# Kernel tuning notes

Hardware: AMD Instinct MI355X
Metric: run time of the kernel (lower is better)

## Reference

```python
import jax, jax.numpy as jnp
import numpy as np

RANK = 16
ALPHA = 32.0
LORA_SCALE = ALPHA / RANK  # 2.0


def setup_inputs() -> dict:
    key = jax.random.key(0)
    ks = jax.random.split(key, 7)
    B_, S, D_IN, D_OUT = 4, 2048, 4096, 4096
    x = jax.random.normal(ks[0], (B_, S, D_IN), dtype=jnp.float32)
    qweight = jax.random.randint(ks[1], (D_OUT, D_IN), 0, 16, dtype=jnp.int32)
    w_min = jax.random.normal(ks[2], (D_OUT, 1), dtype=jnp.float32) * 0.1
    # row scale ~ (max-min)/15 of typical weights; keep positive
    w_scale = jax.random.uniform(ks[3], (D_OUT, 1), dtype=jnp.float32, minval=1e-3, maxval=0.02)
    bias = jax.random.normal(ks[4], (D_OUT,), dtype=jnp.float32) * 0.02
    A = jax.random.normal(ks[5], (RANK, D_IN), dtype=jnp.float32) * 0.02
    # module inits B to zeros; use small randn so the LoRA branch is exercised
    Bm = jax.random.normal(ks[6], (D_OUT, RANK), dtype=jnp.float32) * 0.02
    return {"x": x, "qweight": qweight, "w_min": w_min, "w_scale": w_scale,
            "bias": bias, "A": A, "B": Bm}


def reference(x, qweight, w_min, w_scale, bias, A, B):
    # Row-wise 4-bit dequant: W[o,i] = q[o,i]*scale[o] + min[o]
    base_weight = qweight.astype(jnp.float32) * w_scale + w_min  # [O, I]
    base_out = jnp.einsum('bsi,oi->bso', x, base_weight) + bias   # [B, S, O]
    # LoRA: (x @ A^T) @ B^T * (alpha/rank); dropout p=0 is identity
    lora_out = jnp.einsum('bsr,or->bso', jnp.einsum('bsi,ri->bsr', x, A), B) * LORA_SCALE
    return base_out + lora_out
```

## Files before the change

kernel.cpp:

```cpp
#include <hip/hip_runtime.h>
#include <hip/hip_bf16.h>

typedef unsigned short u16;
typedef unsigned int u32;
typedef __bf16 bf16x8 __attribute__((ext_vector_type(8)));
typedef float f32x4 __attribute__((ext_vector_type(4)));
typedef u16 u16x4 __attribute__((ext_vector_type(4)));
typedef u16 u16x8 __attribute__((ext_vector_type(8)));

#define D_IN 4096
#define D_OUT 4096
#define M_TOT 8192
#define RANK_ 16

#define BM 256
#define BN 256
#define BK 64
#define NT (D_IN / BK)
#define OPB 2

__device__ __forceinline__ u16 f2bf(float f) {
    union { float f; u32 u; } v; v.f = f;
    u32 u = v.u;
    u32 r = (u + 0x7FFFu + ((u >> 16) & 1u)) >> 16;
    return (u16)r;
}

__global__ __launch_bounds__(256) void dequant_fold_kernel(
        const int* __restrict__ q, const float* __restrict__ wmin,
        const float* __restrict__ wscale, const float* __restrict__ A,
        const float* __restrict__ Bm, u16* __restrict__ Wb) {
    const int K = D_IN;
    int o0 = blockIdx.x * OPB;
    float s0 = wscale[o0], s1 = wscale[o0 + 1];
    float m0 = wmin[o0],   m1 = wmin[o0 + 1];
    float Br0[RANK_], Br1[RANK_];
    #pragma unroll
    for (int r = 0; r < RANK_; ++r) {
        Br0[r] = 2.0f * Bm[(size_t)o0 * RANK_ + r];
        Br1[r] = 2.0f * Bm[(size_t)(o0 + 1) * RANK_ + r];
    }
    for (int i4 = threadIdx.x; i4 < K / 4; i4 += 256) {
        int i = i4 * 4;
        int4 q0 = *(const int4*)(q + (size_t)o0 * K + i);
        int4 q1 = *(const int4*)(q + (size_t)(o0 + 1) * K + i);
        float v00 = (float)q0.x * s0 + m0, v01 = (float)q0.y * s0 + m0;
        float v02 = (float)q0.z * s0 + m0, v03 = (float)q0.w * s0 + m0;
        float v10 = (float)q1.x * s1 + m1, v11 = (float)q1.y * s1 + m1;
        float v12 = (float)q1.z * s1 + m1, v13 = (float)q1.w * s1 + m1;
        #pragma unroll
        for (int r = 0; r < RANK_; ++r) {
            float4 av = *(const float4*)(A + (size_t)r * K + i);
            v00 += Br0[r] * av.x; v01 += Br0[r] * av.y;
            v02 += Br0[r] * av.z; v03 += Br0[r] * av.w;
            v10 += Br1[r] * av.x; v11 += Br1[r] * av.y;
            v12 += Br1[r] * av.z; v13 += Br1[r] * av.w;
        }
        u16x4 o0v, o1v;
        o0v.x = f2bf(v00); o0v.y = f2bf(v01); o0v.z = f2bf(v02); o0v.w = f2bf(v03);
        o1v.x = f2bf(v10); o1v.y = f2bf(v11); o1v.z = f2bf(v12); o1v.w = f2bf(v13);
        *(u16x4*)(Wb + (size_t)o0 * K + i) = o0v;
        *(u16x4*)(Wb + (size_t)(o0 + 1) * K + i) = o1v;
    }
}

__global__ void xcast_kernel(const float* __restrict__ x, u16* __restrict__ xb) {
    size_t i = (size_t)blockIdx.x * blockDim.x + threadIdx.x;
    const float4* p = (const float4*)x + i * 2;
    float4 a = p[0];
    float4 b = p[1];
    u16x8 o;
    o[0] = f2bf(a.x); o[1] = f2bf(a.y); o[2] = f2bf(a.z); o[3] = f2bf(a.w);
    o[4] = f2bf(b.x); o[5] = f2bf(b.y); o[6] = f2bf(b.z); o[7] = f2bf(b.w);
    *(u16x8*)(xb + i * 8) = o;
}


#define STAGE2(srcarr, ldsarr, base, j0, kt) do { _Pragma("unroll") \
    for (int j_ = (j0); j_ < (j0) + 2; ++j_) \
        __builtin_amdgcn_global_load_lds( \
            (__attribute__((address_space(1))) u32*)(srcarr[j_] + (kt) * 64), \
            (__attribute__((address_space(3))) u32*)(smem + (base) + ldsarr[j_]), \
            16, 0, 0); } while (0)

#define MFMA(d, va, vb) d = __builtin_amdgcn_mfma_f32_16x16x32_bf16(va, vb, d, 0, 0, 0)

__global__ __launch_bounds__(512, 2) void gemm_bt_kernel(const u16* __restrict__ Xb,
                                                         const u16* __restrict__ Wb,
                                                         const float* __restrict__ bias,
                                                         float* __restrict__ out) {
    extern __shared__ __align__(16) char smem[];
    const int K = D_IN, N = D_OUT;

    int bid = blockIdx.x;
    int swz = (bid & 7) * 64 + (bid >> 3);
    int tM = swz >> 4;
    int tN = swz & 15;

    int t = threadIdx.x;
    int lane = t & 63;
    int wave = t >> 6;
    int wm = wave >> 2;
    int wn = wave & 3;
    int lr = lane & 15;
    int hi = lane >> 4;
    int l7 = lane & 7;

    int xs0 = ((0 * 4 + hi) ^ l7) << 4;
    int xs1 = ((1 * 4 + hi) ^ l7) << 4;
    int aRow = (wm * 128 + lr) * 128;
    int bRow = (wn * 64 + lr) * 128;

    const u16* srcA[4]; const u16* srcB[4]; int ldsA[4]; int ldsB[4];
    {
        int cA[4] = { t, 1024 + t, 512 + t, 1536 + t };
        int b0 = (t & 255) + ((t >> 8) << 9);
        int cB[4] = { b0, b0 + 1024, b0 + 256, b0 + 1280 };
        #pragma unroll
        for (int j = 0; j < 4; ++j) {
            int ca = cA[j], cb = cB[j];
            int rowa = ca >> 3, rowb = cb >> 3;
            int sa = (ca & 7) ^ (rowa & 7);
            int sb = (cb & 7) ^ (rowb & 7);
            srcA[j] = Xb + (size_t)(tM * 256 + rowa) * K + (sa << 3);
            srcB[j] = Wb + (size_t)(tN * 256 + rowb) * K + (sb << 3);
            ldsA[j] = ca * 16;
            ldsB[j] = cb * 16;
        }
    }

    f32x4 acc[8][4];
    #pragma unroll
    for (int i = 0; i < 8; ++i)
        #pragma unroll
        for (int j = 0; j < 4; ++j)
            acc[i][j] = (f32x4){0.f, 0.f, 0.f, 0.f};

    STAGE2(srcA, ldsA, 0,     0, 0); STAGE2(srcA, ldsA, 0,     2, 0);
    STAGE2(srcB, ldsB, 65536, 0, 0); STAGE2(srcB, ldsB, 65536, 2, 0);
    STAGE2(srcA, ldsA, 32768, 0, 1); STAGE2(srcA, ldsA, 32768, 2, 1);
    STAGE2(srcB, ldsB, 98304, 0, 1); STAGE2(srcB, ldsB, 98304, 2, 1);
    asm volatile("s_waitcnt vmcnt(8)" ::: "memory");
    __builtin_amdgcn_s_barrier();

    bf16x8 a[4][2], b[4][2];

    for (int tt = 0; tt < NT; ++tt) {
        int pA = (tt & 1) * 32768;
        int pB = 65536 + (tt & 1) * 32768;
        bool pre = (tt + 2 < NT);

        #pragma unroll
        for (int mf = 0; mf < 4; ++mf) {
            a[mf][0] = *(const bf16x8*)(smem + pA + aRow + mf * 2048 + xs0);
            a[mf][1] = *(const bf16x8*)(smem + pA + aRow + mf * 2048 + xs1);
        }
        #pragma unroll
        for (int nf = 0; nf < 2; ++nf) {
            b[nf][0] = *(const bf16x8*)(smem + pB + bRow + nf * 2048 + xs0);
            b[nf][1] = *(const bf16x8*)(smem + pB + bRow + nf * 2048 + xs1);
        }
        asm volatile("s_waitcnt lgkmcnt(8)" ::: "memory");
        __builtin_amdgcn_s_barrier();
        asm volatile("s_waitcnt lgkmcnt(0)");
        __builtin_amdgcn_s_setprio(1);
        #pragma unroll
        for (int mf = 0; mf < 4; ++mf)
            #pragma unroll
            for (int nf = 0; nf < 2; ++nf) {
                MFMA(acc[mf][nf], a[mf][0], b[nf][0]);
                MFMA(acc[mf][nf], a[mf][1], b[nf][1]);
            }
        __builtin_amdgcn_s_setprio(0);
        __builtin_amdgcn_s_barrier();

        #pragma unroll
        for (int nf = 2; nf < 4; ++nf) {
            b[nf][0] = *(const bf16x8*)(smem + pB + bRow + nf * 2048 + xs0);
            b[nf][1] = *(const bf16x8*)(smem + pB + bRow + nf * 2048 + xs1);
        }
        if (pre) {
            STAGE2(srcA, ldsA, pA, 0, tt + 2);
            STAGE2(srcB, ldsB, pB, 0, tt + 2);
        }
        __builtin_amdgcn_s_barrier();
        asm volatile("s_waitcnt lgkmcnt(0)");
        __builtin_amdgcn_s_setprio(1);
        #pragma unroll
        for (int mf = 0; mf < 4; ++mf)
            #pragma unroll
            for (int nf = 2; nf < 4; ++nf) {
                MFMA(acc[mf][nf], a[mf][0], b[nf][0]);
                MFMA(acc[mf][nf], a[mf][1], b[nf][1]);
            }
        __builtin_amdgcn_s_setprio(0);
        __builtin_amdgcn_s_barrier();

        #pragma unroll
        for (int mf = 0; mf < 4; ++mf) {
            a[mf][0] = *(const bf16x8*)(smem + pA + aRow + (mf + 4) * 2048 + xs0);
            a[mf][1] = *(const bf16x8*)(smem + pA + aRow + (mf + 4) * 2048 + xs1);
        }
        if (pre) { STAGE2(srcB, ldsB, pB, 2, tt + 2); }
        __builtin_amdgcn_s_barrier();
        asm volatile("s_waitcnt lgkmcnt(0)");
        __builtin_amdgcn_s_setprio(1);
        #pragma unroll
        for (int mf = 0; mf < 4; ++mf)
            #pragma unroll
            for (int nf = 2; nf < 4; ++nf) {
                MFMA(acc[mf + 4][nf], a[mf][0], b[nf][0]);
                MFMA(acc[mf + 4][nf], a[mf][1], b[nf][1]);
            }
        __builtin_amdgcn_s_setprio(0);
        __builtin_amdgcn_s_barrier();

        if (pre) { STAGE2(srcA, ldsA, pA, 2, tt + 2); }
        if (tt < NT - 2) { asm volatile("s_waitcnt vmcnt(8)" ::: "memory"); }
        else             { asm volatile("s_waitcnt vmcnt(0)" ::: "memory"); }
        __builtin_amdgcn_s_barrier();
        __builtin_amdgcn_s_setprio(1);
        #pragma unroll
        for (int mf = 0; mf < 4; ++mf)
            #pragma unroll
            for (int nf = 0; nf < 2; ++nf) {
                MFMA(acc[mf + 4][nf], a[mf][0], b[nf][0]);
                MFMA(acc[mf + 4][nf], a[mf][1], b[nf][1]);
            }
        __builtin_amdgcn_s_setprio(0);
        __builtin_amdgcn_s_barrier();
    }

    #pragma unroll
    for (int nf = 0; nf < 4; ++nf) {
        int gn = tN * 256 + wn * 64 + nf * 16 + lr;
        float bs = bias[gn];
        #pragma unroll
        for (int mf = 0; mf < 8; ++mf) {
            #pragma unroll
            for (int r = 0; r < 4; ++r) {
                int gm = tM * 256 + wm * 128 + mf * 16 + hi * 4 + r;
                out[(size_t)gm * N + gn] = acc[mf][nf][r] + bs;
            }
        }
    }
}

extern "C" void kernel_launch(void* const* d_in, const int* in_sizes, int n_in,
                              void* d_out, int out_size, void* d_ws, size_t ws_size,
                              hipStream_t stream) {
    (void)in_sizes; (void)n_in; (void)out_size; (void)ws_size;
    const float* x      = (const float*)d_in[0];
    const int*   qw     = (const int*)d_in[1];
    const float* wmin   = (const float*)d_in[2];
    const float* wscale = (const float*)d_in[3];
    const float* bias   = (const float*)d_in[4];
    const float* A      = (const float*)d_in[5];
    const float* Bm     = (const float*)d_in[6];
    float* out = (float*)d_out;

    u16* Wb = (u16*)d_ws;
    u16* Xb = Wb + (size_t)D_OUT * D_IN;

    dequant_fold_kernel<<<D_OUT / OPB, 256, 0, stream>>>(qw, wmin, wscale, A, Bm, Wb);
    xcast_kernel<<<(M_TOT * D_IN) / (256 * 8), 256, 0, stream>>>(x, Xb);
    gemm_bt_kernel<<<(M_TOT / BM) * (D_OUT / BN), 512, 131072, stream>>>(Xb, Wb, bias, out);
}
```

Measured before the change: 311.8 us.

## Prefetch next tile's B fragments and regroup staging loads by consumer phase

Reorganizes the main GEMM loop so the B columns 0-1 fragments for the next K-tile are read from LDS during the last MFMA phase of the current tile, with ping-pong register sets and the loop unrolled by two. Global-to-LDS staging is regrouped into row ranges (A rows 0-63/64-127 per wave half, B quarter rows) that match the order in which each phase consumes them, so each refill can be issued as soon as its region is free. The aim is to remove the LDS read latency at the start of each tile and tighten the overlap of async copies with MFMA work, at the cost of more live registers and more complex waitcnt reasoning.

```diff
diff --git a/kernel.cpp b/kernel.cpp
--- a/kernel.cpp
+++ b/kernel.cpp
@@ -76,14 +76,104 @@
 }
 
 
-#define STAGE2(srcarr, ldsarr, base, j0, kt) do { _Pragma("unroll") \
-    for (int j_ = (j0); j_ < (j0) + 2; ++j_) \
+#define STAGE_R(sarr, larr, base, kt) do { _Pragma("unroll") \
+    for (int j_ = 0; j_ < 2; ++j_) \
         __builtin_amdgcn_global_load_lds( \
-            (__attribute__((address_space(1))) u32*)(srcarr[j_] + (kt) * 64), \
-            (__attribute__((address_space(3))) u32*)(smem + (base) + ldsarr[j_]), \
+            (__attribute__((address_space(1))) u32*)(sarr[j_] + (kt) * 64), \
+            (__attribute__((address_space(3))) u32*)(smem + (base) + larr[j_]), \
             16, 0, 0); } while (0)
 
 #define MFMA(d, va, vb) d = __builtin_amdgcn_mfma_f32_16x16x32_bf16(va, vb, d, 0, 0, 0)
+
+#define TILE_BODY(tt, BC, BN_) do { \
+    int pA = ((tt) & 1) * 32768; \
+    int pB = 65536 + ((tt) & 1) * 32768; \
+    int pBn = 65536 + ((~(tt)) & 1) * 32768; \
+    bool pre = ((tt) + 2 < NT); \
+     \
+    _Pragma("unroll") \
+    for (int mf = 0; mf < 4; ++mf) { \
+        a[mf][0] = *(const bf16x8*)(smem + pA + aRow + mf * 2048 + xs0); \
+        a[mf][1] = *(const bf16x8*)(smem + pA + aRow + mf * 2048 + xs1); \
+    } \
+    if (pre && (tt) > 0) { STAGE_R(srcB01, ldsB01, pB, (tt) + 2); } \
+    __builtin_amdgcn_s_barrier(); \
+    asm volatile("s_waitcnt lgkmcnt(0)"); \
+    __builtin_amdgcn_s_setprio(1); \
+    _Pragma("unroll") \
+    for (int mf = 0; mf < 4; ++mf) \
+        _Pragma("unroll") \
+        for (int nf = 0; nf < 2; ++nf) { \
+            MFMA(acc[mf][nf], a[mf][0], BC[nf][0]); \
+            MFMA(acc[mf][nf], a[mf][1], BC[nf][1]); \
+        } \
+    __builtin_amdgcn_s_setprio(0); \
+    __builtin_amdgcn_s_barrier(); \
+     \
+    _Pragma("unroll") \
+    for (int nf = 0; nf < 2; ++nf) { \
+        b23[nf][0] = *(const bf16x8*)(smem + pB + bRow + (nf + 2) * 2048 + xs0); \
+        b23[nf][1] = *(const bf16x8*)(smem + pB + bRow + (nf + 2) * 2048 + xs1); \
+    } \
+    if (pre) { \
+        STAGE_R(srcA03, ldsA03, pA, (tt) + 2); \
+        if ((tt) == 0) { STAGE_R(srcB01, ldsB01, pB, (tt) + 2); } \
+    } \
+    __builtin_amdgcn_s_barrier(); \
+    asm volatile("s_waitcnt lgkmcnt(0)"); \
+    __builtin_amdgcn_s_setprio(1); \
+    _Pragma("unroll") \
+    for (int mf = 0; mf < 4; ++mf) \
+        _Pragma("unroll") \
+        for (int nf = 0; nf < 2; ++nf) { \
+            MFMA(acc[mf][nf + 2], a[mf][0], b23[nf][0]); \
+            MFMA(acc[mf][nf + 2], a[mf][1], b23[nf][1]); \
+        } \
+    __builtin_amdgcn_s_setprio(0); \
+    __builtin_amdgcn_s_barrier(); \
+     \
+    _Pragma("unroll") \
+    for (int mf = 0; mf < 4; ++mf) { \
+        a[mf][0] = *(const bf16x8*)(smem + pA + aRow + (mf + 4) * 2048 + xs0); \
+        a[mf][1] = *(const bf16x8*)(smem + pA + aRow + (mf + 4) * 2048 + xs1); \
+    } \
+    if (pre) { STAGE_R(srcB23, ldsB23, pB, (tt) + 2); } \
+    __builtin_amdgcn_s_barrier(); \
+    asm volatile("s_waitcnt lgkmcnt(0)"); \
+    __builtin_amdgcn_s_setprio(1); \
+    _Pragma("unroll") \
+    for (int mf = 0; mf < 4; ++mf) \
+        _Pragma("unroll") \
+        for (int nf = 0; nf < 2; ++nf) { \
+            MFMA(acc[mf + 4][nf + 2], a[mf][0], b23[nf][0]); \
+            MFMA(acc[mf + 4][nf + 2], a[mf][1], b23[nf][1]); \
+        } \
+    __builtin_amdgcn_s_setprio(0); \
+    __builtin_amdgcn_s_barrier(); \
+     \
+     \
+    if (pre) { STAGE_R(srcA47, ldsA47, pA, (tt) + 2); } \
+    if ((tt) < NT - 2) { asm volatile("s_waitcnt vmcnt(8)" ::: "memory"); } \
+    else               { asm volatile("s_waitcnt vmcnt(0)" ::: "memory"); } \
+    __builtin_amdgcn_s_barrier(); \
+    if ((tt) + 1 < NT) { \
+        _Pragma("unroll") \
+        for (int nf = 0; nf < 2; ++nf) { \
+            BN_[nf][0] = *(const bf16x8*)(smem + pBn + bRow + nf * 2048 + xs0); \
+            BN_[nf][1] = *(const bf16x8*)(smem + pBn + bRow + nf * 2048 + xs1); \
+        } \
+    } \
+    __builtin_amdgcn_s_setprio(1); \
+    _Pragma("unroll") \
+    for (int mf = 0; mf < 4; ++mf) \
+        _Pragma("unroll") \
+        for (int nf = 0; nf < 2; ++nf) { \
+            MFMA(acc[mf + 4][nf], a[mf][0], BC[nf][0]); \
+            MFMA(acc[mf + 4][nf], a[mf][1], BC[nf][1]); \
+        } \
+    __builtin_amdgcn_s_setprio(0); \
+    __builtin_amdgcn_s_barrier(); \
+} while (0)
 
 __global__ __launch_bounds__(512, 2) void gemm_bt_kernel(const u16* __restrict__ Xb,
                                                          const u16* __restrict__ Wb,
@@ -111,22 +201,26 @@
     int aRow = (wm * 128 + lr) * 128;
     int bRow = (wn * 64 + lr) * 128;
 
-    const u16* srcA[4]; const u16* srcB[4]; int ldsA[4]; int ldsB[4];
-    {
-        int cA[4] = { t, 1024 + t, 512 + t, 1536 + t };
-        int b0 = (t & 255) + ((t >> 8) << 9);
-        int cB[4] = { b0, b0 + 1024, b0 + 256, b0 + 1280 };
-        #pragma unroll
-        for (int j = 0; j < 4; ++j) {
-            int ca = cA[j], cb = cB[j];
-            int rowa = ca >> 3, rowb = cb >> 3;
-            int sa = (ca & 7) ^ (rowa & 7);
-            int sb = (cb & 7) ^ (rowb & 7);
-            srcA[j] = Xb + (size_t)(tM * 256 + rowa) * K + (sa << 3);
-            srcB[j] = Wb + (size_t)(tN * 256 + rowb) * K + (sb << 3);
-            ldsA[j] = ca * 16;
-            ldsB[j] = cb * 16;
-        }
+    const u16 *srcA03[2], *srcA47[2], *srcB01[2], *srcB23[2];
+    int ldsA03[2], ldsA47[2], ldsB01[2], ldsB23[2];
+    #pragma unroll
+    for (int j = 0; j < 2; ++j) {
+        int idx = j * 512 + t;
+        int rl = idx >> 3, slot = idx & 7;
+        int rA = (rl & 63) + ((rl >> 6) << 7);
+        int rB = (rl & 31) + ((rl >> 5) << 6);
+        int r = rA;
+        ldsA03[j] = r * 128 + slot * 16;
+        srcA03[j] = Xb + (size_t)(tM * 256 + r) * K + ((slot ^ (r & 7)) << 3);
+        r = rA + 64;
+        ldsA47[j] = r * 128 + slot * 16;
+        srcA47[j] = Xb + (size_t)(tM * 256 + r) * K + ((slot ^ (r & 7)) << 3);
+        r = rB;
+        ldsB01[j] = r * 128 + slot * 16;
+        srcB01[j] = Wb + (size_t)(tN * 256 + r) * K + ((slot ^ (r & 7)) << 3);
+        r = rB + 32;
+        ldsB23[j] = r * 128 + slot * 16;
+        srcB23[j] = Wb + (size_t)(tN * 256 + r) * K + ((slot ^ (r & 7)) << 3);
     }
 
     f32x4 acc[8][4];
@@ -136,99 +230,23 @@
         for (int j = 0; j < 4; ++j)
             acc[i][j] = (f32x4){0.f, 0.f, 0.f, 0.f};
 
-    STAGE2(srcA, ldsA, 0,     0, 0); STAGE2(srcA, ldsA, 0,     2, 0);
-    STAGE2(srcB, ldsB, 65536, 0, 0); STAGE2(srcB, ldsB, 65536, 2, 0);
-    STAGE2(srcA, ldsA, 32768, 0, 1); STAGE2(srcA, ldsA, 32768, 2, 1);
-    STAGE2(srcB, ldsB, 98304, 0, 1); STAGE2(srcB, ldsB, 98304, 2, 1);
+    STAGE_R(srcA03, ldsA03, 0, 0);     STAGE_R(srcA47, ldsA47, 0, 0);
+    STAGE_R(srcB01, ldsB01, 65536, 0); STAGE_R(srcB23, ldsB23, 65536, 0);
+    STAGE_R(srcA03, ldsA03, 32768, 1); STAGE_R(srcA47, ldsA47, 32768, 1);
+    STAGE_R(srcB01, ldsB01, 98304, 1); STAGE_R(srcB23, ldsB23, 98304, 1);
     asm volatile("s_waitcnt vmcnt(8)" ::: "memory");
     __builtin_amdgcn_s_barrier();
 
-    bf16x8 a[4][2], b[4][2];
-
-    for (int tt = 0; tt < NT; ++tt) {
-        int pA = (tt & 1) * 32768;
-        int pB = 65536 + (tt & 1) * 32768;
-        bool pre = (tt + 2 < NT);
-
-        #pragma unroll
-        for (int mf = 0; mf < 4; ++mf) {
-            a[mf][0] = *(const bf16x8*)(smem + pA + aRow + mf * 2048 + xs0);
-            a[mf][1] = *(const bf16x8*)(smem + pA + aRow + mf * 2048 + xs1);
-        }
-        #pragma unroll
-        for (int nf = 0; nf < 2; ++nf) {
-            b[nf][0] = *(const bf16x8*)(smem + pB + bRow + nf * 2048 + xs0);
-            b[nf][1] = *(const bf16x8*)(smem + pB + bRow + nf * 2048 + xs1);
-        }
-        asm volatile("s_waitcnt lgkmcnt(8)" ::: "memory");
-        __builtin_amdgcn_s_barrier();
-        asm volatile("s_waitcnt lgkmcnt(0)");
-        __builtin_amdgcn_s_setprio(1);
-        #pragma unroll
-        for (int mf = 0; mf < 4; ++mf)
-            #pragma unroll
-            for (int nf = 0; nf < 2; ++nf) {
-                MFMA(acc[mf][nf], a[mf][0], b[nf][0]);
-                MFMA(acc[mf][nf], a[mf][1], b[nf][1]);
-            }
-        __builtin_amdgcn_s_setprio(0);
-        __builtin_amdgcn_s_barrier();
-
-        #pragma unroll
-        for (int nf = 2; nf < 4; ++nf) {
-            b[nf][0] = *(const bf16x8*)(smem + pB + bRow + nf * 2048 + xs0);
-            b[nf][1] = *(const bf16x8*)(smem + pB + bRow + nf * 2048 + xs1);
-        }
-        if (pre) {
-            STAGE2(srcA, ldsA, pA, 0, tt + 2);
-            STAGE2(srcB, ldsB, pB, 0, tt + 2);
-        }
-        __builtin_amdgcn_s_barrier();
-        asm volatile("s_waitcnt lgkmcnt(0)");
-        __builtin_amdgcn_s_setprio(1);
-        #pragma unroll
-        for (int mf = 0; mf < 4; ++mf)
-            #pragma unroll
-            for (int nf = 2; nf < 4; ++nf) {
-                MFMA(acc[mf][nf], a[mf][0], b[nf][0]);
-                MFMA(acc[mf][nf], a[mf][1], b[nf][1]);
-            }
-        __builtin_amdgcn_s_setprio(0);
-        __builtin_amdgcn_s_barrier();
-
-        #pragma unroll
-        for (int mf = 0; mf < 4; ++mf) {
-            a[mf][0] = *(const bf16x8*)(smem + pA + aRow + (mf + 4) * 2048 + xs0);
-            a[mf][1] = *(const bf16x8*)(smem + pA + aRow + (mf + 4) * 2048 + xs1);
-        }
-        if (pre) { STAGE2(srcB, ldsB, pB, 2, tt + 2); }
-        __builtin_amdgcn_s_barrier();
-        asm volatile("s_waitcnt lgkmcnt(0)");
-        __builtin_amdgcn_s_setprio(1);
-        #pragma unroll
-        for (int mf = 0; mf < 4; ++mf)
-            #pragma unroll
-            for (int nf = 2; nf < 4; ++nf) {
-                MFMA(acc[mf + 4][nf], a[mf][0], b[nf][0]);
-                MFMA(acc[mf + 4][nf], a[mf][1], b[nf][1]);
-            }
-        __builtin_amdgcn_s_setprio(0);
-        __builtin_amdgcn_s_barrier();
-
-        if (pre) { STAGE2(srcA, ldsA, pA, 2, tt + 2); }
-        if (tt < NT - 2) { asm volatile("s_waitcnt vmcnt(8)" ::: "memory"); }
-        else             { asm volatile("s_waitcnt vmcnt(0)" ::: "memory"); }
-        __builtin_amdgcn_s_barrier();
-        __builtin_amdgcn_s_setprio(1);
-        #pragma unroll
-        for (int mf = 0; mf < 4; ++mf)
-            #pragma unroll
-            for (int nf = 0; nf < 2; ++nf) {
-                MFMA(acc[mf + 4][nf], a[mf][0], b[nf][0]);
-                MFMA(acc[mf + 4][nf], a[mf][1], b[nf][1]);
-            }
-        __builtin_amdgcn_s_setprio(0);
-        __builtin_amdgcn_s_barrier();
+    bf16x8 a[4][2], b23[2][2], b01A[2][2], b01B[2][2];
+    #pragma unroll
+    for (int nf = 0; nf < 2; ++nf) {
+        b01A[nf][0] = *(const bf16x8*)(smem + 65536 + bRow + nf * 2048 + xs0);
+        b01A[nf][1] = *(const bf16x8*)(smem + 65536 + bRow + nf * 2048 + xs1);
+    }
+
+    for (int tt = 0; tt < NT; tt += 2) {
+        TILE_BODY(tt, b01A, b01B);
+        TILE_BODY(tt + 1, b01B, b01A);
     }
 
     #pragma unroll
```

After: 362.4 us. +16.2%, slower.

## Prefetch next-tile B fragments across iterations and regroup LDS staging by row halves

Applied to the files above, without the earlier changes.

Splits the B register fragments into b01/b23 and loads the next iteration's b01 during the final MFMA phase, so each iteration's first MFMA block no longer waits on B reads from LDS. The global-to-LDS staging is regrouped so each stage copies a contiguous half of the A or B rows (A rows 0-63/64-127 per wave half, B column groups 0-1/2-3). The MFMA phase order is changed to match which data has landed. This adds register pressure for the extra fragments and makes the barrier and waitcnt ordering more delicate.

```diff
diff --git a/kernel.cpp b/kernel.cpp
--- a/kernel.cpp
+++ b/kernel.cpp
@@ -76,11 +76,11 @@
 }
 
 
-#define STAGE2(srcarr, ldsarr, base, j0, kt) do { _Pragma("unroll") \
-    for (int j_ = (j0); j_ < (j0) + 2; ++j_) \
+#define STAGE_R(sarr, larr, base, kt) do { _Pragma("unroll") \
+    for (int j_ = 0; j_ < 2; ++j_) \
         __builtin_amdgcn_global_load_lds( \
-            (__attribute__((address_space(1))) u32*)(srcarr[j_] + (kt) * 64), \
-            (__attribute__((address_space(3))) u32*)(smem + (base) + ldsarr[j_]), \
+            (__attribute__((address_space(1))) u32*)(sarr[j_] + (kt) * 64), \
+            (__attribute__((address_space(3))) u32*)(smem + (base) + larr[j_]), \
             16, 0, 0); } while (0)
 
 #define MFMA(d, va, vb) d = __builtin_amdgcn_mfma_f32_16x16x32_bf16(va, vb, d, 0, 0, 0)
@@ -111,22 +111,26 @@
     int aRow = (wm * 128 + lr) * 128;
     int bRow = (wn * 64 + lr) * 128;
 
-    const u16* srcA[4]; const u16* srcB[4]; int ldsA[4]; int ldsB[4];
-    {
-        int cA[4] = { t, 1024 + t, 512 + t, 1536 + t };
-        int b0 = (t & 255) + ((t >> 8) << 9);
-        int cB[4] = { b0, b0 + 1024, b0 + 256, b0 + 1280 };
-        #pragma unroll
-        for (int j = 0; j < 4; ++j) {
-            int ca = cA[j], cb = cB[j];
-            int rowa = ca >> 3, rowb = cb >> 3;
-            int sa = (ca & 7) ^ (rowa & 7);
-            int sb = (cb & 7) ^ (rowb & 7);
-            srcA[j] = Xb + (size_t)(tM * 256 + rowa) * K + (sa << 3);
-            srcB[j] = Wb + (size_t)(tN * 256 + rowb) * K + (sb << 3);
-            ldsA[j] = ca * 16;
-            ldsB[j] = cb * 16;
-        }
+    const u16 *srcA03[2], *srcA47[2], *srcB01[2], *srcB23[2];
+    int ldsA03[2], ldsA47[2], ldsB01[2], ldsB23[2];
+    #pragma unroll
+    for (int j = 0; j < 2; ++j) {
+        int idx = j * 512 + t;
+        int rl = idx >> 3, slot = idx & 7;
+        int rA = (rl & 63) + ((rl >> 6) << 7);
+        int rB = (rl & 31) + ((rl >> 5) << 6);
+        int r = rA;
+        ldsA03[j] = r * 128 + slot * 16;
+        srcA03[j] = Xb + (size_t)(tM * 256 + r) * K + ((slot ^ (r & 7)) << 3);
+        r = rA + 64;
+        ldsA47[j] = r * 128 + slot * 16;
+        srcA47[j] = Xb + (size_t)(tM * 256 + r) * K + ((slot ^ (r & 7)) << 3);
+        r = rB;
+        ldsB01[j] = r * 128 + slot * 16;
+        srcB01[j] = Wb + (size_t)(tN * 256 + r) * K + ((slot ^ (r & 7)) << 3);
+        r = rB + 32;
+        ldsB23[j] = r * 128 + slot * 16;
+        srcB23[j] = Wb + (size_t)(tN * 256 + r) * K + ((slot ^ (r & 7)) << 3);
     }
 
     f32x4 acc[8][4];
@@ -136,18 +140,24 @@
         for (int j = 0; j < 4; ++j)
             acc[i][j] = (f32x4){0.f, 0.f, 0.f, 0.f};
 
-    STAGE2(srcA, ldsA, 0,     0, 0); STAGE2(srcA, ldsA, 0,     2, 0);
-    STAGE2(srcB, ldsB, 65536, 0, 0); STAGE2(srcB, ldsB, 65536, 2, 0);
-    STAGE2(srcA, ldsA, 32768, 0, 1); STAGE2(srcA, ldsA, 32768, 2, 1);
-    STAGE2(srcB, ldsB, 98304, 0, 1); STAGE2(srcB, ldsB, 98304, 2, 1);
+    STAGE_R(srcA03, ldsA03, 0, 0);     STAGE_R(srcA47, ldsA47, 0, 0);
+    STAGE_R(srcB01, ldsB01, 65536, 0); STAGE_R(srcB23, ldsB23, 65536, 0);
+    STAGE_R(srcA03, ldsA03, 32768, 1); STAGE_R(srcA47, ldsA47, 32768, 1);
+    STAGE_R(srcB01, ldsB01, 98304, 1); STAGE_R(srcB23, ldsB23, 98304, 1);
     asm volatile("s_waitcnt vmcnt(8)" ::: "memory");
     __builtin_amdgcn_s_barrier();
 
-    bf16x8 a[4][2], b[4][2];
+    bf16x8 a[4][2], b23[2][2], b01[2][2];
+    #pragma unroll
+    for (int nf = 0; nf < 2; ++nf) {
+        b01[nf][0] = *(const bf16x8*)(smem + 65536 + bRow + nf * 2048 + xs0);
+        b01[nf][1] = *(const bf16x8*)(smem + 65536 + bRow + nf * 2048 + xs1);
+    }
 
     for (int tt = 0; tt < NT; ++tt) {
         int pA = (tt & 1) * 32768;
         int pB = 65536 + (tt & 1) * 32768;
+        int pBn = 65536 + ((~tt) & 1) * 32768;
         bool pre = (tt + 2 < NT);
 
         #pragma unroll
@@ -155,12 +165,29 @@
             a[mf][0] = *(const bf16x8*)(smem + pA + aRow + mf * 2048 + xs0);
             a[mf][1] = *(const bf16x8*)(smem + pA + aRow + mf * 2048 + xs1);
         }
+        asm volatile("s_waitcnt lgkmcnt(4)" ::: "memory");
+        __builtin_amdgcn_s_barrier();
+        asm volatile("s_waitcnt lgkmcnt(0)");
+        __builtin_amdgcn_s_setprio(1);
+        #pragma unroll
+        for (int mf = 0; mf < 4; ++mf)
+            #pragma unroll
+            for (int nf = 0; nf < 2; ++nf) {
+                MFMA(acc[mf][nf], a[mf][0], b01[nf][0]);
+                MFMA(acc[mf][nf], a[mf][1], b01[nf][1]);
+            }
+        __builtin_amdgcn_s_setprio(0);
+        __builtin_amdgcn_s_barrier();
+
         #pragma unroll
         for (int nf = 0; nf < 2; ++nf) {
-            b[nf][0] = *(const bf16x8*)(smem + pB + bRow + nf * 2048 + xs0);
-            b[nf][1] = *(const bf16x8*)(smem + pB + bRow + nf * 2048 + xs1);
-        }
-        asm volatile("s_waitcnt lgkmcnt(8)" ::: "memory");
+            b23[nf][0] = *(const bf16x8*)(smem + pB + bRow + (nf + 2) * 2048 + xs0);
+            b23[nf][1] = *(const bf16x8*)(smem + pB + bRow + (nf + 2) * 2048 + xs1);
+        }
+        if (pre) {
+            STAGE_R(srcA03, ldsA03, pA, tt + 2);
+            STAGE_R(srcB01, ldsB01, pB, tt + 2);
+        }
         __builtin_amdgcn_s_barrier();
         asm volatile("s_waitcnt lgkmcnt(0)");
         __builtin_amdgcn_s_setprio(1);
@@ -168,30 +195,8 @@
         for (int mf = 0; mf < 4; ++mf)
             #pragma unroll
             for (int nf = 0; nf < 2; ++nf) {
-                MFMA(acc[mf][nf], a[mf][0], b[nf][0]);
-                MFMA(acc[mf][nf], a[mf][1], b[nf][1]);
-            }
-        __builtin_amdgcn_s_setprio(0);
-        __builtin_amdgcn_s_barrier();
-
-        #pragma unroll
-        for (int nf = 2; nf < 4; ++nf) {
-            b[nf][0] = *(const bf16x8*)(smem + pB + bRow + nf * 2048 + xs0);
-            b[nf][1] = *(const bf16x8*)(smem + pB + bRow + nf * 2048 + xs1);
-        }
-        if (pre) {
-            STAGE2(srcA, ldsA, pA, 0, tt + 2);
-            STAGE2(srcB, ldsB, pB, 0, tt + 2);
-        }
-        __builtin_amdgcn_s_barrier();
-        asm volatile("s_waitcnt lgkmcnt(0)");
-        __builtin_amdgcn_s_setprio(1);
-        #pragma unroll
-        for (int mf = 0; mf < 4; ++mf)
-            #pragma unroll
-            for (int nf = 2; nf < 4; ++nf) {
-                MFMA(acc[mf][nf], a[mf][0], b[nf][0]);
-                MFMA(acc[mf][nf], a[mf][1], b[nf][1]);
+                MFMA(acc[mf][nf + 2], a[mf][0], b23[nf][0]);
+                MFMA(acc[mf][nf + 2], a[mf][1], b23[nf][1]);
             }
         __builtin_amdgcn_s_setprio(0);
         __builtin_amdgcn_s_barrier();
@@ -201,31 +206,39 @@
             a[mf][0] = *(const bf16x8*)(smem + pA + aRow + (mf + 4) * 2048 + xs0);
             a[mf][1] = *(const bf16x8*)(smem + pA + aRow + (mf + 4) * 2048 + xs1);
         }
-        if (pre) { STAGE2(srcB, ldsB, pB, 2, tt + 2); }
+        if (pre) { STAGE_R(srcB23, ldsB23, pB, tt + 2); }
+        asm volatile("s_waitcnt lgkmcnt(4)" ::: "memory");
         __builtin_amdgcn_s_barrier();
         asm volatile("s_waitcnt lgkmcnt(0)");
         __builtin_amdgcn_s_setprio(1);
         #pragma unroll
         for (int mf = 0; mf < 4; ++mf)
             #pragma unroll
-            for (int nf = 2; nf < 4; ++nf) {
-                MFMA(acc[mf + 4][nf], a[mf][0], b[nf][0]);
-                MFMA(acc[mf + 4][nf], a[mf][1], b[nf][1]);
-            }
-        __builtin_amdgcn_s_setprio(0);
-        __builtin_amdgcn_s_barrier();
-
-        if (pre) { STAGE2(srcA, ldsA, pA, 2, tt + 2); }
+            for (int nf = 0; nf < 2; ++nf) {
+                MFMA(acc[mf + 4][nf], a[mf][0], b01[nf][0]);
+                MFMA(acc[mf + 4][nf], a[mf][1], b01[nf][1]);
+            }
+        __builtin_amdgcn_s_setprio(0);
+        __builtin_amdgcn_s_barrier();
+
+        if (pre) { STAGE_R(srcA47, ldsA47, pA, tt + 2); }
         if (tt < NT - 2) { asm volatile("s_waitcnt vmcnt(8)" ::: "memory"); }
         else             { asm volatile("s_waitcnt vmcnt(0)" ::: "memory"); }
         __builtin_amdgcn_s_barrier();
-        __builtin_amdgcn_s_setprio(1);
-        #pragma unroll
-        for (int mf = 0; mf < 4; ++mf)
-            #pragma unroll
-            for (int nf = 0; nf < 2; ++nf) {
-                MFMA(acc[mf + 4][nf], a[mf][0], b[nf][0]);
-                MFMA(acc[mf + 4][nf], a[mf][1], b[nf][1]);
+        if (tt + 1 < NT) {
+            #pragma unroll
+            for (int nf = 0; nf < 2; ++nf) {
+                b01[nf][0] = *(const bf16x8*)(smem + pBn + bRow + nf * 2048 + xs0);
+                b01[nf][1] = *(const bf16x8*)(smem + pBn + bRow + nf * 2048 + xs1);
+            }
+        }
+        __builtin_amdgcn_s_setprio(1);
+        #pragma unroll
+        for (int mf = 0; mf < 4; ++mf)
+            #pragma unroll
+            for (int nf = 0; nf < 2; ++nf) {
+                MFMA(acc[mf + 4][nf + 2], a[mf][0], b23[nf][0]);
+                MFMA(acc[mf + 4][nf + 2], a[mf][1], b23[nf][1]);
             }
         __builtin_amdgcn_s_setprio(0);
         __builtin_amdgcn_s_barrier();
```

New measurement: 302.6 us. 1.03x faster.
